# Kernel tuning notes

Hardware: AMD Instinct MI355X
Metric: run time of the kernel (lower is better)

Reference implementation:

```python
import jax, jax.numpy as jnp
import numpy as np
import math

N = 50000   # nodes
E = 800000  # edges
D = 128     # in/out dim
T = 4       # node types
H = 8       # heads (forced: Linear(8,64).view(-1, H, 8))
DK = D // H
HD = 8      # h_mat feature dim


def setup_inputs() -> dict:
    key = jax.random.key(0)
    ks = jax.random.split(key, 16)
    g = lambda k, shp, fan: jax.random.uniform(k, shp, jnp.float32, -1.0, 1.0) * math.sqrt(6.0 / fan)
    return {
        "meta_xs": jax.random.normal(ks[0], (N, D), jnp.float32),
        "node_type": jax.random.randint(ks[1], (N,), 0, T),
        "edge_index": jax.random.randint(ks[2], (2, E), 0, N),
        "h_mat": jax.random.normal(ks[3], (N, HD), jnp.float32),
        "sub_W": g(ks[4], (T, D, D), 2 * D),
        "sub_b": jnp.zeros((T, D), jnp.float32),
        "neigh_W": g(ks[5], (T, D, D), 2 * D),
        "neigh_b": jnp.zeros((T, D), jnp.float32),
        "hsub_W": g(ks[6], (HD, H * HD), HD + H * HD),
        "hsub_b": jnp.zeros((H * HD,), jnp.float32),
        "hneigh_W": g(ks[7], (HD, H * HD), HD + H * HD),
        "hneigh_b": jnp.zeros((H * HD,), jnp.float32),
        "relation_att": g(ks[8], (T, H, DK), H + DK),
        "relation_h_att": g(ks[9], (T, H, HD), H + HD),
        "ln_gamma": jnp.ones((D,), jnp.float32),
        "ln_beta": jnp.zeros((D,), jnp.float32),
    }


def _hgt_forward(meta_xs, h_mat, sub_W, sub_b, neigh_W, neigh_b, hsub_W, hsub_b,
                 hneigh_W, hneigh_b, relation_att, relation_h_att, ln_gamma, ln_beta,
                 node_type, edge_index):
    n = meta_xs.shape[0]
    e = edge_index.shape[1]
    src = edge_index[0]  # edge_index_j (neighbor)
    dst = edge_index[1]  # edge_index_i (sub / target)
    sqrt_dk = math.sqrt(DK)
    d_h = math.sqrt(H)

    # per-node, type-selected linear projections (sub by own type, neigh by own type)
    q_all = jnp.einsum('nd,tdo->tno', meta_xs, sub_W) + sub_b[:, None, :]      # [T,N,D]
    k_all = jnp.einsum('nd,tdo->tno', meta_xs, neigh_W) + neigh_b[:, None, :]  # [T,N,D]
    ar = jnp.arange(n)
    q_node = q_all[node_type, ar]  # [N,D] sub_linear[type_i](x_i)
    k_node = k_all[node_type, ar]  # [N,D] neigh_linear[type_j](x_j)

    h_sub_node = (h_mat @ hsub_W + hsub_b).reshape(n, H, HD)
    h_neigh_node = (h_mat @ hneigh_W + hneigh_b).reshape(n, H, HD)

    st = node_type[dst]  # sub type per edge selects relation params
    h_s = h_sub_node[dst]    # [E,H,8]
    h_n = h_neigh_node[src]  # [E,H,8]
    att_h = jnp.sum(jnp.tanh(h_s * h_n) * relation_h_att[st], axis=-1) / d_h  # [E,H]

    q_e = q_node[dst].reshape(e, H, DK)
    k_e = k_node[src].reshape(e, H, DK)
    att = jnp.sum(jnp.tanh(q_e * k_e) * relation_att[st], axis=-1) / sqrt_dk * att_h  # [E,H]

    # edge softmax over destination segments
    m = jax.ops.segment_max(att, dst, num_segments=n)  # [N,H]
    ea = jnp.exp(att - m[dst])
    denom = jax.ops.segment_sum(ea, dst, num_segments=n)
    alpha = ea / (denom[dst] + 1e-16)  # [E,H]

    msg = (k_e * alpha[:, :, None]).reshape(e, D)
    aggr = jax.ops.segment_sum(msg, dst, num_segments=n)  # [N,D]

    out = jax.nn.gelu(aggr, approximate=False)
    mu = jnp.mean(out, axis=-1, keepdims=True)
    var = jnp.var(out, axis=-1, keepdims=True)
    return (out - mu) * jax.lax.rsqrt(var + 1e-5) * ln_gamma + ln_beta


def reference(meta_xs, node_type, edge_index, h_mat, sub_W, sub_b, neigh_W, neigh_b,
              hsub_W, hsub_b, hneigh_W, hneigh_b, relation_att, relation_h_att,
              ln_gamma, ln_beta):
    return _hgt_forward(meta_xs, h_mat, sub_W, sub_b, neigh_W, neigh_b, hsub_W, hsub_b,
                        hneigh_W, hneigh_b, relation_att, relation_h_att, ln_gamma, ln_beta,
                        node_type, edge_index)
```

## Files before the change

kernel.cpp:

```cpp
#include <hip/hip_runtime.h>

typedef __bf16 bf16x8 __attribute__((ext_vector_type(8)));
typedef float f32x4 __attribute__((ext_vector_type(4)));

#define B_CHUNK 64
#define R_RANGE 2

__device__ __forceinline__ float exp2_fast(float x){
#if __has_builtin(__builtin_amdgcn_exp2f)
  return __builtin_amdgcn_exp2f(x);
#else
  return __expf(x * 0.69314718055994531f);
#endif
}
template<int CTRL>
__device__ __forceinline__ float dpp_add(float x){
  union { float f; int i; } a, b;
  a.f = x;
  b.i = __builtin_amdgcn_mov_dpp(a.i, CTRL, 0xF, 0xF, true);
  return x + b.f;
}
__device__ __forceinline__ float sum4(float x){
  x = dpp_add<0xB1>(x);
  x = dpp_add<0x4E>(x);
  return x;
}
__device__ __forceinline__ unsigned int cvt_pk_bf16(float lo, float hi){
  unsigned int r;
  asm("v_cvt_pk_bf16_f32 %0, %1, %2" : "=v"(r) : "v"(lo), "v"(hi));
  return r;
}
__device__ __forceinline__ unsigned short f2bf1(float f){
  return (unsigned short)cvt_pk_bf16(f, f);
}
__device__ __forceinline__ bf16x8 ld_bf8(const unsigned short* p){
  union { uint4 u; bf16x8 v; } c;
  c.u = *reinterpret_cast<const uint4*>(p);
  return c.v;
}
__device__ __forceinline__ bf16x8 ld_f32_to_bf8(const float* p){
  float4 lo = *reinterpret_cast<const float4*>(p);
  float4 hi = *reinterpret_cast<const float4*>(p + 4);
  union { unsigned int u[4]; bf16x8 v; } c;
  c.u[0] = cvt_pk_bf16(lo.x, lo.y);
  c.u[1] = cvt_pk_bf16(lo.z, lo.w);
  c.u[2] = cvt_pk_bf16(hi.x, hi.y);
  c.u[3] = cvt_pk_bf16(hi.z, hi.w);
  return c.v;
}

__global__ __launch_bounds__(256) void k_prep(const int* ntype, int* tcur, int* nbt,
                       int Npad, int N,
                       const float* subW, const float* neighW,
                       unsigned short* wts, unsigned short* wtn,
                       const int* ei, int E, unsigned short* hist,
                       unsigned short* rank, int RNG, int HR, int NB){
  __shared__ unsigned int lsh[12544];
  int b = blockIdx.x;
  const int SB1 = B_CHUNK * R_RANGE;
  if (b < SB1){
    int cb = b & (B_CHUNK - 1);
    int r  = b >> 6;
    int lo = r * RNG;
    int bins = RNG >> 1;
    for (int i = threadIdx.x; i < bins; i += 256) lsh[i] = 0;
    __syncthreads();
    int C = (E + B_CHUNK - 1) / B_CHUNK;
    int e0 = cb * C;
    int e1 = e0 + C; if (e1 > E) e1 = E;
    for (int i = e0 + threadIdx.x; i < e1; i += 256){
      int d = ei[E + i] - lo;
      if ((unsigned)d < (unsigned)RNG){
        unsigned old = atomicAdd(&lsh[d >> 1], (d & 1) ? 65536u : 1u);
        rank[i] = (unsigned short)((old >> ((d & 1) << 4)) & 0xffffu);
      }
    }
    __syncthreads();
    unsigned int* hrow = reinterpret_cast<unsigned int*>(hist + (size_t)cb*HR + lo);
    for (int i = threadIdx.x; i < bins; i += 256) hrow[i] = lsh[i];
  } else if (b < SB1 + NB){
    int i = (b - SB1)*256 + threadIdx.x;
    if (i >= N) return;
    int lane = threadIdx.x & 63;
    int myt = ntype[i];
    unsigned long long below = (lane == 0) ? 0ull : ((~0ull) >> (64 - lane));
    #pragma unroll
    for (int tt = 0; tt < 4; ++tt){
      unsigned long long mask = __ballot(myt == tt);
      if (mask){
        int leader = __ffsll((long long)mask) - 1;
        int base = 0;
        if (lane == leader) base = atomicAdd(&tcur[tt], __popcll(mask));
        base = __shfl(base, leader);
        if (myt == tt){
          int pos = base + __popcll(mask & below);
          nbt[tt*Npad + pos] = i;
        }
      }
    }
  } else {
    int i = (b - SB1 - NB)*256 + threadIdx.x;
    int w = i >> 16;
    int r = i & 65535;
    int t = r >> 14;
    int rem = r & 16383;
    int o = rem >> 7;
    int kd = rem & 127;
    const float* src = w ? neighW : subW;
    unsigned short* dstp = w ? wtn : wts;
    dstp[(t << 14) + (o << 7) + kd] = f2bf1(src[(t << 14) + (kd << 7) + o]);
  }
}

__global__ __launch_bounds__(256) void k_mid(unsigned short* hist, int HR,
                       int* deg, int N, int SCB,
                       const float* h_mat, const float* hsW, const float* hsb,
                       const float* hnW, const float* hnb,
                       float2* hs2, char* hnc){
  int b = blockIdx.x;
  if (b < SCB){
    int d = b*256 + threadIdx.x;
    if (d >= N) return;
    unsigned run = 0;
    #pragma unroll 4
    for (int c = 0; c < B_CHUNK; ++c){
      unsigned short* p = hist + (size_t)c*HR + d;
      unsigned v = *p;
      *p = (unsigned short)run;
      run += v;
    }
    deg[d] = (int)run;
  } else {
    int i = (b - SCB)*256 + threadIdx.x;
    if (i >= N*32) return;
    int n = i >> 5, l = i & 31;
    const float* hm = h_mat + (size_t)n*8;
    const float2* hsW2 = reinterpret_cast<const float2*>(hsW);
    const float2* hnW2 = reinterpret_cast<const float2*>(hnW);
    float s0=0.f, s1=0.f, n0=0.f, n1=0.f;
    #pragma unroll
    for (int d = 0; d < 8; ++d){
      float hv = hm[d];
      float2 ws2 = hsW2[d*32 + l];
      float2 wn2 = hnW2[d*32 + l];
      s0 += hv * ws2.x; s1 += hv * ws2.y;
      n0 += hv * wn2.x; n1 += hv * wn2.y;
    }
    float2 bs = reinterpret_cast<const float2*>(hsb)[l];
    float2 bn = reinterpret_cast<const float2*>(hnb)[l];
    hs2[(size_t)i] = make_float2(s0 + bs.x, s1 + bs.y);
    *reinterpret_cast<unsigned int*>(hnc + (size_t)n*128 + l*4)
        = cvt_pk_bf16(n0 + bn.x, n1 + bn.y);
  }
}

__global__ __launch_bounds__(256) void k_ms(const float* X,
      const unsigned short* wts, const unsigned short* wtn,
      const float* sub_b, const float* neigh_b,
      const int* nbt, const int* tcur, int Npad,
      float* q, char* kkc,
      const int* ei, unsigned short* bucket, int E,
      const unsigned short* hist, int HR, const unsigned short* rank, int MB){
  int b = blockIdx.x;
  if (b < MB){
    int t = -1, chunk = 0, acc = 0;
    #pragma unroll
    for (int tt = 0; tt < 4; ++tt){
      int cnt = tcur[tt];
      int nc = (cnt + 63) >> 6;
      if (t < 0 && b < acc + nc){ t = tt; chunk = b - acc; }
      acc += nc;
    }
    if (t < 0) return;
    int lane = threadIdx.x & 63;
    int w = threadIdx.x >> 6;
    int quad = lane >> 4, l16 = lane & 15;
    int cnt = tcur[t];
    int p = chunk*64 + w*16 + l16;
    bool ok = p < cnt;
    int nid = nbt[t*Npad + (ok ? p : 0)];
    bf16x8 xb[4];
    #pragma unroll
    for (int kk = 0; kk < 4; ++kk)
      xb[kk] = ld_f32_to_bf8(X + (size_t)nid*128 + kk*32 + quad*8);
    #pragma unroll
    for (int pj = 0; pj < 2; ++pj){
      const unsigned short* Wt = pj ? wtn : wts;
      const float* bias = pj ? neigh_b : sub_b;
      #pragma unroll
      for (int ot = 0; ot < 8; ++ot){
        f32x4 c = {0.f, 0.f, 0.f, 0.f};
        #pragma unroll
        for (int kk = 0; kk < 4; ++kk){
          bf16x8 wa = ld_bf8(Wt + ((size_t)t << 14) + ((size_t)(ot*16 + l16) << 7)
                                + kk*32 + quad*8);
          c = __builtin_amdgcn_mfma_f32_16x16x32_bf16(wa, xb[kk], c, 0, 0, 0);
        }
        int o0 = ot*16 + quad*4;
        float4 b4 = *reinterpret_cast<const float4*>(bias + t*128 + o0);
        if (ok){
          if (pj == 0){
            float4 v = make_float4(c[0]+b4.x, c[1]+b4.y, c[2]+b4.z, c[3]+b4.w);
            *reinterpret_cast<float4*>(q + (size_t)nid*128 + o0) = v;
          } else {
            uint2 pk;
            pk.x = cvt_pk_bf16(c[0]+b4.x, c[1]+b4.y);
            pk.y = cvt_pk_bf16(c[2]+b4.z, c[3]+b4.w);
            *reinterpret_cast<uint2*>(kkc + ((size_t)nid << 8) + (size_t)(o0 << 1)) = pk;
          }
        }
      }
    }
  } else {
    int sb = b - MB;
    int cb = sb >> 3;
    int sub = sb & 7;
    int C = (E + B_CHUNK - 1) / B_CHUNK;
    int seg = (C + 7) >> 3;
    int s0 = sub*seg;
    int s1 = s0 + seg; if (s1 > C) s1 = C;
    int e0 = cb*C + s0;
    int e1 = cb*C + s1; if (e1 > E) e1 = E;
    const unsigned short* hrow = hist + (size_t)cb*HR;
    for (int i = e0 + threadIdx.x; i < e1; i += 256){
      int d = ei[E + i];
      int pos = (int)hrow[d] + (int)rank[i];
      if (pos < 128) bucket[(size_t)d*128 + pos] = (unsigned short)ei[i];
    }
  }
}

__global__ __launch_bounds__(256) void k_edge(const float* q, const char* kkc,
      const char* hnc, const float2* hs2, const int* degA,
      const unsigned short* bucket, const int* ntype,
      const float* rel_att, const float* rel_h_att,
      const float* ln_g, const float* ln_b,
      float* out, int N){
  int wid = (blockIdx.x*blockDim.x + threadIdx.x) >> 6;
  if (wid >= N) return;
  int lane = threadIdx.x & 63;
  int l = lane & 31;
  int half = (lane >> 5) & 1;
  int t4 = l & 3, head = l >> 2;
  const float TLOG2E = 2.8853900817779268f;
  float4 qv = *reinterpret_cast<const float4*>(q + (size_t)wid*128 + l*4);
  float qe0 = qv.x*TLOG2E, qe1 = qv.y*TLOG2E, qe2 = qv.z*TLOG2E, qe3 = qv.w*TLOG2E;
  float2 hv = hs2[(size_t)wid*32 + l];
  float he0 = hv.x*TLOG2E, he1 = hv.y*TLOG2E;
  int st = ntype[wid];
  int rb = st*8 + head;
  float4 ra = *reinterpret_cast<const float4*>(rel_att + rb*16 + t4*4);
  float2 rh = *reinterpret_cast<const float2*>(rel_h_att + rb*8 + t4*2);
  float c0 = -0.5f*ra.x, c1 = -0.5f*ra.y, c2 = -0.5f*ra.z, c3 = -0.5f*ra.w;
  float cs = 0.25f*(ra.x + ra.y + ra.z + ra.w);
  const float HSC = 0.35355339059327373f * 1.4426950408889634f;
  float rh0 = rh.x*HSC, rh1 = rh.y*HSC;
  float ch0 = -2.f*rh0, ch1 = -2.f*rh1, chs = rh0 + rh1;
  float s = 0.f, a0 = 0.f, a1 = 0.f, a2 = 0.f, a3 = 0.f;

  int deg = __builtin_amdgcn_readfirstlane(degA[wid]);
  if (deg > 128) deg = 128;
  unsigned bkt = reinterpret_cast<const unsigned*>(bucket)[(size_t)wid*64 + lane];
  int niter = (deg + 1) >> 1;
  const char* kk_l = kkc + l*8;
  const char* hn_l = hnc + l*4;

  struct KH { uint2 k; unsigned h; };
  auto lp = [&](int g)->KH {
    int gg = g < niter ? g : 0;
    unsigned v = (unsigned)__builtin_amdgcn_readlane((int)bkt, gg);
    int sA = (int)(v & 0xffffu);
    int sB = (2*gg + 1 < deg) ? (int)(v >> 16) : sA;
    int sy = half ? sB : sA;
    KH r;
    r.k = *reinterpret_cast<const uint2*>(kk_l + ((size_t)(unsigned)sy << 8));
    r.h = *reinterpret_cast<const unsigned*>(hn_l + ((size_t)(unsigned)sy << 7));
    return r;
  };
  auto pr = [&](KH P, int g){
    union { unsigned u; float f; } k0,k1,k2,k3,h0,h1;
    k0.u = P.k.x << 16; k1.u = P.k.x & 0xffff0000u;
    k2.u = P.k.y << 16; k3.u = P.k.y & 0xffff0000u;
    h0.u = P.h << 16;   h1.u = P.h & 0xffff0000u;
    float e0 = exp2_fast(qe0*k0.f), e1 = exp2_fast(qe1*k1.f);
    float e2 = exp2_fast(qe2*k2.f), e3 = exp2_fast(qe3*k3.f);
    float f0 = exp2_fast(he0*h0.f), f1 = exp2_fast(he1*h1.f);
    float r0 = __builtin_amdgcn_rcpf(e0 + 1.f), r1 = __builtin_amdgcn_rcpf(e1 + 1.f);
    float r2 = __builtin_amdgcn_rcpf(e2 + 1.f), r3 = __builtin_amdgcn_rcpf(e3 + 1.f);
    float g0 = __builtin_amdgcn_rcpf(f0 + 1.f), g1 = __builtin_amdgcn_rcpf(f1 + 1.f);
    float pp = fmaf(c0,r0, fmaf(c1,r1, fmaf(c2,r2, fmaf(c3,r3, cs))));
    float ph = fmaf(ch0,g0, fmaf(ch1,g1, chs));
    pp = sum4(pp);
    ph = sum4(ph);
    float w = exp2_fast(pp * ph);
    w = (2*g + half < deg) ? w : 0.f;
    s += w;
    a0 = fmaf(w, k0.f, a0); a1 = fmaf(w, k1.f, a1);
    a2 = fmaf(w, k2.f, a2); a3 = fmaf(w, k3.f, a3);
  };

  if (niter > 0){
    KH A = lp(0);
    KH B = lp(1);
    for (int g = 0; g < niter; g += 2){
      KH C = lp(g+2);
      pr(A, g);
      KH D = lp(g+3);
      if (g+1 < niter) pr(B, g+1);
      A = C; B = D;
    }
  }
  s  += __shfl_xor(s, 32);
  a0 += __shfl_xor(a0, 32); a1 += __shfl_xor(a1, 32);
  a2 += __shfl_xor(a2, 32); a3 += __shfl_xor(a3, 32);

  float inv = 1.0f / (s + 1e-16f);
  float x0 = a0*inv, x1 = a1*inv, x2 = a2*inv, x3 = a3*inv;
  const float IS2 = 0.70710678118654752f;
  x0 = 0.5f*x0*(1.f + erff(x0*IS2));
  x1 = 0.5f*x1*(1.f + erff(x1*IS2));
  x2 = 0.5f*x2*(1.f + erff(x2*IS2));
  x3 = 0.5f*x3*(1.f + erff(x3*IS2));
  float sm = x0+x1+x2+x3;
  float sq = x0*x0 + x1*x1 + x2*x2 + x3*x3;
  #pragma unroll
  for (int d = 1; d < 32; d <<= 1){ sm += __shfl_xor(sm, d); sq += __shfl_xor(sq, d); }
  float mu = sm * (1.f/128.f);
  float var = fmaxf(sq * (1.f/128.f) - mu*mu, 0.f);
  float r = rsqrtf(var + 1e-5f);
  if (half == 0){
    float4 g4 = *reinterpret_cast<const float4*>(ln_g + l*4);
    float4 b4 = *reinterpret_cast<const float4*>(ln_b + l*4);
    float4 o4 = make_float4((x0-mu)*r*g4.x + b4.x, (x1-mu)*r*g4.y + b4.y,
                            (x2-mu)*r*g4.z + b4.z, (x3-mu)*r*g4.w + b4.w);
    *reinterpret_cast<float4*>(out + (size_t)wid*128 + l*4) = o4;
  }
}

extern "C" void kernel_launch(void* const* d_in, const int* in_sizes, int n_in,
                              void* d_out, int out_size, void* d_ws, size_t ws_size,
                              hipStream_t stream) {
  const float* meta_xs  = (const float*)d_in[0];
  const int*   node_type= (const int*)d_in[1];
  const int*   edge_idx = (const int*)d_in[2];
  const float* h_mat    = (const float*)d_in[3];
  const float* sub_W    = (const float*)d_in[4];
  const float* sub_b    = (const float*)d_in[5];
  const float* neigh_W  = (const float*)d_in[6];
  const float* neigh_b  = (const float*)d_in[7];
  const float* hsub_W   = (const float*)d_in[8];
  const float* hsub_b   = (const float*)d_in[9];
  const float* hneigh_W = (const float*)d_in[10];
  const float* hneigh_b = (const float*)d_in[11];
  const float* rel_att  = (const float*)d_in[12];
  const float* rel_hatt = (const float*)d_in[13];
  const float* ln_g     = (const float*)d_in[14];
  const float* ln_b     = (const float*)d_in[15];

  const int N = in_sizes[0] / 128;
  const int E = in_sizes[2] / 2;
  const int Npad = (N + 63) & ~63;
  const int RNG = (((N + R_RANGE - 1) / R_RANGE) + 1) & ~1;
  const int HR  = RNG * R_RANGE;

  char* wbase = (char*)d_ws;
  size_t o = 0;
  auto carve = [&](size_t bytes)->char* {
    char* p = wbase + o;
    o = (o + bytes + 255) & ~(size_t)255;
    return p;
  };
  float*          q      = (float*)carve((size_t)N*128*4);
  char*           kkc    = carve((size_t)N*256);
  char*           hnc    = carve((size_t)N*128);
  float2*         hs2    = (float2*)carve((size_t)N*32*8);
  unsigned short* bucket = (unsigned short*)carve((size_t)N*128*2);
  unsigned short* hist   = (unsigned short*)carve((size_t)B_CHUNK*HR*2);
  unsigned short* rank   = (unsigned short*)carve((size_t)E*2);
  int*            deg    = (int*)carve((size_t)N*4);
  int*            tmeta  = (int*)carve(64);
  int*            nbt    = (int*)carve((size_t)4*Npad*4);
  unsigned short* wts    = (unsigned short*)carve((size_t)4*128*128*2);
  unsigned short* wtn    = (unsigned short*)carve((size_t)4*128*128*2);
  if (o > ws_size) return;

  int* tcur = tmeta;

  const int SB1 = B_CHUNK * R_RANGE;
  const int NB  = (N + 255) / 256;
  const int WB  = (2*4*128*128) / 256;
  const int SCB = (N + 255) / 256;
  const int HB  = (N*32 + 255) / 256;
  const int MB  = ((N + 63) >> 6) + 4;
  const int SB3 = B_CHUNK * 8;

  hipMemsetAsync(tmeta, 0, 64, stream);
  k_prep <<<SB1 + NB + WB, 256, 0, stream>>>(node_type, tcur, nbt, Npad, N,
                                       sub_W, neigh_W, wts, wtn,
                                       edge_idx, E, hist, rank, RNG, HR, NB);
  k_mid  <<<SCB + HB, 256, 0, stream>>>(hist, HR, deg, N, SCB,
                                       h_mat, hsub_W, hsub_b, hneigh_W, hneigh_b,
                                       hs2, hnc);
  k_ms   <<<MB + SB3, 256, 0, stream>>>(meta_xs, wts, wtn, sub_b, neigh_b,
                                       nbt, tcur, Npad, q, kkc,
                                       edge_idx, bucket, E, hist, HR, rank, MB);
  k_edge <<<(N+3)/4, 256, 0, stream>>>(q, kkc, hnc, hs2, deg, bucket, node_type,
                                       rel_att, rel_hatt, ln_g, ln_b,
                                       (float*)d_out, N);
}
```

Baseline: 291.8 us.

## Fuse preprocessing kernels into one cooperative persistent kernel with grid syncs

Merges the three preprocessing launches and the memset into a single cooperative kernel of 768 blocks. Work is rebalanced across phases separated by grid-wide syncs, and type bucketing moves to after the histogram phase. R_RANGE goes from 2 to 4 so the histogram shared buffer halves, which allows more blocks to be resident for a cooperative launch. The aim is to cut launch gaps and tail effects, at the cost of grid-sync overhead and more histogram passes over the edges. Separate kernels remain as a fallback if the cooperative launch fails.

```diff
diff --git a/kernel.cpp b/kernel.cpp
--- a/kernel.cpp
+++ b/kernel.cpp
@@ -1,10 +1,14 @@
 #include <hip/hip_runtime.h>
+#include <hip/hip_cooperative_groups.h>
+
+namespace cg = cooperative_groups;
 
 typedef __bf16 bf16x8 __attribute__((ext_vector_type(8)));
 typedef float f32x4 __attribute__((ext_vector_type(4)));
 
 #define B_CHUNK 64
-#define R_RANGE 2
+#define R_RANGE 4
+#define GRID_F 768
 
 __device__ __forceinline__ float exp2_fast(float x){
 #if __has_builtin(__builtin_amdgcn_exp2f)
@@ -49,186 +53,216 @@
   return c.v;
 }
 
-__global__ __launch_bounds__(256) void k_prep(const int* ntype, int* tcur, int* nbt,
-                       int Npad, int N,
-                       const float* subW, const float* neighW,
-                       unsigned short* wts, unsigned short* wtn,
-                       const int* ei, int E, unsigned short* hist,
-                       unsigned short* rank, int RNG, int HR, int NB){
-  __shared__ unsigned int lsh[12544];
-  int b = blockIdx.x;
+struct FArgs {
+  const int* ntype; int* tcur; int* nbt; int Npad; int N;
+  const float* subW; const float* neighW;
+  unsigned short* wts; unsigned short* wtn;
+  const int* ei; int E;
+  unsigned short* hist; unsigned short* rank; int RNG; int HR;
+  const float* h_mat; const float* hsW; const float* hsb;
+  const float* hnW; const float* hnb;
+  float2* hs2; char* hnc;
+  const float* X; const float* sub_b; const float* neigh_b;
+  float* q; char* kkc;
+  unsigned short* bucket; int* deg;
+};
+
+__device__ void phaseA(const FArgs& a, int bid, int nb){
+  __shared__ unsigned int lsh[6272];
   const int SB1 = B_CHUNK * R_RANGE;
-  if (b < SB1){
-    int cb = b & (B_CHUNK - 1);
-    int r  = b >> 6;
-    int lo = r * RNG;
-    int bins = RNG >> 1;
-    for (int i = threadIdx.x; i < bins; i += 256) lsh[i] = 0;
-    __syncthreads();
-    int C = (E + B_CHUNK - 1) / B_CHUNK;
-    int e0 = cb * C;
-    int e1 = e0 + C; if (e1 > E) e1 = E;
-    for (int i = e0 + threadIdx.x; i < e1; i += 256){
-      int d = ei[E + i] - lo;
-      if ((unsigned)d < (unsigned)RNG){
-        unsigned old = atomicAdd(&lsh[d >> 1], (d & 1) ? 65536u : 1u);
-        rank[i] = (unsigned short)((old >> ((d & 1) << 4)) & 0xffffu);
+  const int WB  = 512;
+  const int HB  = (a.N*32 + 255) >> 8;
+  const int TA  = SB1 + WB + HB;
+  if (bid == 0 && threadIdx.x < 4) a.tcur[threadIdx.x] = 0;
+  for (int t = bid; t < TA; t += nb){
+    if (t < SB1){
+      int cb = t & (B_CHUNK - 1);
+      int r  = t >> 6;
+      int lo = r * a.RNG;
+      int bins = a.RNG >> 1;
+      __syncthreads();
+      for (int i = threadIdx.x; i < bins; i += 256) lsh[i] = 0;
+      __syncthreads();
+      int C = (a.E + B_CHUNK - 1) / B_CHUNK;
+      int e0 = cb * C;
+      int e1 = e0 + C; if (e1 > a.E) e1 = a.E;
+      for (int i = e0 + threadIdx.x; i < e1; i += 256){
+        int d = a.ei[a.E + i] - lo;
+        if ((unsigned)d < (unsigned)a.RNG){
+          unsigned old = atomicAdd(&lsh[d >> 1], (d & 1) ? 65536u : 1u);
+          a.rank[i] = (unsigned short)((old >> ((d & 1) << 4)) & 0xffffu);
+        }
+      }
+      __syncthreads();
+      unsigned int* hrow =
+          reinterpret_cast<unsigned int*>(a.hist + (size_t)cb*a.HR + lo);
+      for (int i = threadIdx.x; i < bins; i += 256) hrow[i] = lsh[i];
+      __syncthreads();
+    } else if (t < SB1 + WB){
+      int i = (t - SB1)*256 + threadIdx.x;
+      int w = i >> 16;
+      int r = i & 65535;
+      int tt = r >> 14;
+      int rem = r & 16383;
+      int o = rem >> 7;
+      int kd = rem & 127;
+      const float* src = w ? a.neighW : a.subW;
+      unsigned short* dstp = w ? a.wtn : a.wts;
+      dstp[(tt << 14) + (o << 7) + kd] = f2bf1(src[(tt << 14) + (kd << 7) + o]);
+    } else {
+      int i = (t - SB1 - WB)*256 + threadIdx.x;
+      if (i < a.N*32){
+        int n = i >> 5, l = i & 31;
+        const float* hm = a.h_mat + (size_t)n*8;
+        const float2* hsW2 = reinterpret_cast<const float2*>(a.hsW);
+        const float2* hnW2 = reinterpret_cast<const float2*>(a.hnW);
+        float s0=0.f, s1=0.f, n0=0.f, n1=0.f;
+        #pragma unroll
+        for (int d = 0; d < 8; ++d){
+          float hv = hm[d];
+          float2 ws2 = hsW2[d*32 + l];
+          float2 wn2 = hnW2[d*32 + l];
+          s0 += hv * ws2.x; s1 += hv * ws2.y;
+          n0 += hv * wn2.x; n1 += hv * wn2.y;
+        }
+        float2 bs = reinterpret_cast<const float2*>(a.hsb)[l];
+        float2 bn = reinterpret_cast<const float2*>(a.hnb)[l];
+        a.hs2[(size_t)i] = make_float2(s0 + bs.x, s1 + bs.y);
+        *reinterpret_cast<unsigned int*>(a.hnc + (size_t)n*128 + l*4)
+            = cvt_pk_bf16(n0 + bn.x, n1 + bn.y);
       }
     }
-    __syncthreads();
-    unsigned int* hrow = reinterpret_cast<unsigned int*>(hist + (size_t)cb*HR + lo);
-    for (int i = threadIdx.x; i < bins; i += 256) hrow[i] = lsh[i];
-  } else if (b < SB1 + NB){
-    int i = (b - SB1)*256 + threadIdx.x;
-    if (i >= N) return;
-    int lane = threadIdx.x & 63;
-    int myt = ntype[i];
-    unsigned long long below = (lane == 0) ? 0ull : ((~0ull) >> (64 - lane));
-    #pragma unroll
-    for (int tt = 0; tt < 4; ++tt){
-      unsigned long long mask = __ballot(myt == tt);
-      if (mask){
-        int leader = __ffsll((long long)mask) - 1;
-        int base = 0;
-        if (lane == leader) base = atomicAdd(&tcur[tt], __popcll(mask));
-        base = __shfl(base, leader);
-        if (myt == tt){
-          int pos = base + __popcll(mask & below);
-          nbt[tt*Npad + pos] = i;
+  }
+}
+
+__device__ void phaseB(const FArgs& a, int bid, int nb){
+  const int SCB = (a.N + 255) >> 8;
+  const int TB  = SCB * 2;
+  for (int t = bid; t < TB; t += nb){
+    if (t < SCB){
+      int d = t*256 + threadIdx.x;
+      if (d < a.N){
+        unsigned run = 0;
+        #pragma unroll 4
+        for (int c = 0; c < B_CHUNK; ++c){
+          unsigned short* p = a.hist + (size_t)c*a.HR + d;
+          unsigned v = *p;
+          *p = (unsigned short)run;
+          run += v;
         }
-      }
-    }
-  } else {
-    int i = (b - SB1 - NB)*256 + threadIdx.x;
-    int w = i >> 16;
-    int r = i & 65535;
-    int t = r >> 14;
-    int rem = r & 16383;
-    int o = rem >> 7;
-    int kd = rem & 127;
-    const float* src = w ? neighW : subW;
-    unsigned short* dstp = w ? wtn : wts;
-    dstp[(t << 14) + (o << 7) + kd] = f2bf1(src[(t << 14) + (kd << 7) + o]);
-  }
-}
-
-__global__ __launch_bounds__(256) void k_mid(unsigned short* hist, int HR,
-                       int* deg, int N, int SCB,
-                       const float* h_mat, const float* hsW, const float* hsb,
-                       const float* hnW, const float* hnb,
-                       float2* hs2, char* hnc){
-  int b = blockIdx.x;
-  if (b < SCB){
-    int d = b*256 + threadIdx.x;
-    if (d >= N) return;
-    unsigned run = 0;
-    #pragma unroll 4
-    for (int c = 0; c < B_CHUNK; ++c){
-      unsigned short* p = hist + (size_t)c*HR + d;
-      unsigned v = *p;
-      *p = (unsigned short)run;
-      run += v;
-    }
-    deg[d] = (int)run;
-  } else {
-    int i = (b - SCB)*256 + threadIdx.x;
-    if (i >= N*32) return;
-    int n = i >> 5, l = i & 31;
-    const float* hm = h_mat + (size_t)n*8;
-    const float2* hsW2 = reinterpret_cast<const float2*>(hsW);
-    const float2* hnW2 = reinterpret_cast<const float2*>(hnW);
-    float s0=0.f, s1=0.f, n0=0.f, n1=0.f;
-    #pragma unroll
-    for (int d = 0; d < 8; ++d){
-      float hv = hm[d];
-      float2 ws2 = hsW2[d*32 + l];
-      float2 wn2 = hnW2[d*32 + l];
-      s0 += hv * ws2.x; s1 += hv * ws2.y;
-      n0 += hv * wn2.x; n1 += hv * wn2.y;
-    }
-    float2 bs = reinterpret_cast<const float2*>(hsb)[l];
-    float2 bn = reinterpret_cast<const float2*>(hnb)[l];
-    hs2[(size_t)i] = make_float2(s0 + bs.x, s1 + bs.y);
-    *reinterpret_cast<unsigned int*>(hnc + (size_t)n*128 + l*4)
-        = cvt_pk_bf16(n0 + bn.x, n1 + bn.y);
-  }
-}
-
-__global__ __launch_bounds__(256) void k_ms(const float* X,
-      const unsigned short* wts, const unsigned short* wtn,
-      const float* sub_b, const float* neigh_b,
-      const int* nbt, const int* tcur, int Npad,
-      float* q, char* kkc,
-      const int* ei, unsigned short* bucket, int E,
-      const unsigned short* hist, int HR, const unsigned short* rank, int MB){
-  int b = blockIdx.x;
-  if (b < MB){
-    int t = -1, chunk = 0, acc = 0;
-    #pragma unroll
-    for (int tt = 0; tt < 4; ++tt){
-      int cnt = tcur[tt];
-      int nc = (cnt + 63) >> 6;
-      if (t < 0 && b < acc + nc){ t = tt; chunk = b - acc; }
-      acc += nc;
-    }
-    if (t < 0) return;
-    int lane = threadIdx.x & 63;
-    int w = threadIdx.x >> 6;
-    int quad = lane >> 4, l16 = lane & 15;
-    int cnt = tcur[t];
-    int p = chunk*64 + w*16 + l16;
-    bool ok = p < cnt;
-    int nid = nbt[t*Npad + (ok ? p : 0)];
-    bf16x8 xb[4];
-    #pragma unroll
-    for (int kk = 0; kk < 4; ++kk)
-      xb[kk] = ld_f32_to_bf8(X + (size_t)nid*128 + kk*32 + quad*8);
-    #pragma unroll
-    for (int pj = 0; pj < 2; ++pj){
-      const unsigned short* Wt = pj ? wtn : wts;
-      const float* bias = pj ? neigh_b : sub_b;
-      #pragma unroll
-      for (int ot = 0; ot < 8; ++ot){
-        f32x4 c = {0.f, 0.f, 0.f, 0.f};
+        a.deg[d] = (int)run;
+      }
+    } else {
+      int i = (t - SCB)*256 + threadIdx.x;
+      if (i < a.N){
+        int lane = threadIdx.x & 63;
+        int myt = a.ntype[i];
+        unsigned long long below = (lane == 0) ? 0ull : ((~0ull) >> (64 - lane));
         #pragma unroll
-        for (int kk = 0; kk < 4; ++kk){
-          bf16x8 wa = ld_bf8(Wt + ((size_t)t << 14) + ((size_t)(ot*16 + l16) << 7)
-                                + kk*32 + quad*8);
-          c = __builtin_amdgcn_mfma_f32_16x16x32_bf16(wa, xb[kk], c, 0, 0, 0);
-        }
-        int o0 = ot*16 + quad*4;
-        float4 b4 = *reinterpret_cast<const float4*>(bias + t*128 + o0);
-        if (ok){
-          if (pj == 0){
-            float4 v = make_float4(c[0]+b4.x, c[1]+b4.y, c[2]+b4.z, c[3]+b4.w);
-            *reinterpret_cast<float4*>(q + (size_t)nid*128 + o0) = v;
-          } else {
-            uint2 pk;
-            pk.x = cvt_pk_bf16(c[0]+b4.x, c[1]+b4.y);
-            pk.y = cvt_pk_bf16(c[2]+b4.z, c[3]+b4.w);
-            *reinterpret_cast<uint2*>(kkc + ((size_t)nid << 8) + (size_t)(o0 << 1)) = pk;
+        for (int tt = 0; tt < 4; ++tt){
+          unsigned long long mask = __ballot(myt == tt);
+          if (mask){
+            int leader = __ffsll((long long)mask) - 1;
+            int base = 0;
+            if (lane == leader) base = atomicAdd(&a.tcur[tt], __popcll(mask));
+            base = __shfl(base, leader);
+            if (myt == tt){
+              int pos = base + __popcll(mask & below);
+              a.nbt[tt*a.Npad + pos] = i;
+            }
           }
         }
       }
     }
-  } else {
-    int sb = b - MB;
-    int cb = sb >> 3;
-    int sub = sb & 7;
-    int C = (E + B_CHUNK - 1) / B_CHUNK;
-    int seg = (C + 7) >> 3;
-    int s0 = sub*seg;
-    int s1 = s0 + seg; if (s1 > C) s1 = C;
-    int e0 = cb*C + s0;
-    int e1 = cb*C + s1; if (e1 > E) e1 = E;
-    const unsigned short* hrow = hist + (size_t)cb*HR;
-    for (int i = e0 + threadIdx.x; i < e1; i += 256){
-      int d = ei[E + i];
-      int pos = (int)hrow[d] + (int)rank[i];
-      if (pos < 128) bucket[(size_t)d*128 + pos] = (unsigned short)ei[i];
+  }
+}
+
+__device__ void phaseC(const FArgs& a, int bid, int nb){
+  const int SB3 = 512;
+  const int MBX = ((a.N + 63) >> 6) + 4;
+  const int TC  = SB3 + MBX;
+  for (int t = bid; t < TC; t += nb){
+    if (t < SB3){
+      int cb = t >> 3;
+      int sub = t & 7;
+      int C = (a.E + B_CHUNK - 1) / B_CHUNK;
+      int seg = (C + 7) >> 3;
+      int s0 = sub*seg;
+      int s1 = s0 + seg; if (s1 > C) s1 = C;
+      int e0 = cb*C + s0;
+      int e1 = cb*C + s1; if (e1 > a.E) e1 = a.E;
+      const unsigned short* hrow = a.hist + (size_t)cb*a.HR;
+      for (int i = e0 + threadIdx.x; i < e1; i += 256){
+        int d = a.ei[a.E + i];
+        int pos = (int)hrow[d] + (int)a.rank[i];
+        if (pos < 128) a.bucket[(size_t)d*128 + pos] = (unsigned short)a.ei[i];
+      }
+    } else {
+      int b = t - SB3;
+      int ts = -1, chunk = 0, acc = 0;
+      #pragma unroll
+      for (int tt = 0; tt < 4; ++tt){
+        int cnt = a.tcur[tt];
+        int nc = (cnt + 63) >> 6;
+        if (ts < 0 && b < acc + nc){ ts = tt; chunk = b - acc; }
+        acc += nc;
+      }
+      if (ts >= 0){
+        int lane = threadIdx.x & 63;
+        int w = threadIdx.x >> 6;
+        int quad = lane >> 4, l16 = lane & 15;
+        int cnt = a.tcur[ts];
+        int p = chunk*64 + w*16 + l16;
+        bool ok = p < cnt;
+        int nid = a.nbt[ts*a.Npad + (ok ? p : 0)];
+        bf16x8 xb[4];
+        #pragma unroll
+        for (int kk = 0; kk < 4; ++kk)
+          xb[kk] = ld_f32_to_bf8(a.X + (size_t)nid*128 + kk*32 + quad*8);
+        #pragma unroll
+        for (int pj = 0; pj < 2; ++pj){
+          const unsigned short* Wt = pj ? a.wtn : a.wts;
+          const float* bias = pj ? a.neigh_b : a.sub_b;
+          #pragma unroll
+          for (int ot = 0; ot < 8; ++ot){
+            f32x4 c = {0.f, 0.f, 0.f, 0.f};
+            #pragma unroll
+            for (int kk = 0; kk < 4; ++kk){
+              bf16x8 wa = ld_bf8(Wt + ((size_t)ts << 14) + ((size_t)(ot*16 + l16) << 7)
+                                    + kk*32 + quad*8);
+              c = __builtin_amdgcn_mfma_f32_16x16x32_bf16(wa, xb[kk], c, 0, 0, 0);
+            }
+            int o0 = ot*16 + quad*4;
+            float4 b4 = *reinterpret_cast<const float4*>(bias + ts*128 + o0);
+            if (ok){
+              if (pj == 0){
+                float4 v = make_float4(c[0]+b4.x, c[1]+b4.y, c[2]+b4.z, c[3]+b4.w);
+                *reinterpret_cast<float4*>(a.q + (size_t)nid*128 + o0) = v;
+              } else {
+                uint2 pk;
+                pk.x = cvt_pk_bf16(c[0]+b4.x, c[1]+b4.y);
+                pk.y = cvt_pk_bf16(c[2]+b4.z, c[3]+b4.w);
+                *reinterpret_cast<uint2*>(a.kkc + ((size_t)nid << 8) + (size_t)(o0 << 1)) = pk;
+              }
+            }
+          }
+        }
+      }
     }
   }
 }
+
+__global__ __launch_bounds__(256) void k_all(FArgs a){
+  cg::grid_group g = cg::this_grid();
+  phaseA(a, blockIdx.x, gridDim.x);
+  g.sync();
+  phaseB(a, blockIdx.x, gridDim.x);
+  g.sync();
+  phaseC(a, blockIdx.x, gridDim.x);
+}
+__global__ __launch_bounds__(256) void kA(FArgs a){ phaseA(a, blockIdx.x, gridDim.x); }
+__global__ __launch_bounds__(256) void kB(FArgs a){ phaseB(a, blockIdx.x, gridDim.x); }
+__global__ __launch_bounds__(256) void kC(FArgs a){ phaseC(a, blockIdx.x, gridDim.x); }
 
 __global__ __launch_bounds__(256) void k_edge(const float* q, const char* kkc,
       const char* hnc, const float2* hs2, const int* degA,
@@ -384,27 +418,28 @@
   unsigned short* wtn    = (unsigned short*)carve((size_t)4*128*128*2);
   if (o > ws_size) return;
 
-  int* tcur = tmeta;
-
-  const int SB1 = B_CHUNK * R_RANGE;
-  const int NB  = (N + 255) / 256;
-  const int WB  = (2*4*128*128) / 256;
-  const int SCB = (N + 255) / 256;
-  const int HB  = (N*32 + 255) / 256;
-  const int MB  = ((N + 63) >> 6) + 4;
-  const int SB3 = B_CHUNK * 8;
-
-  hipMemsetAsync(tmeta, 0, 64, stream);
-  k_prep <<<SB1 + NB + WB, 256, 0, stream>>>(node_type, tcur, nbt, Npad, N,
-                                       sub_W, neigh_W, wts, wtn,
-                                       edge_idx, E, hist, rank, RNG, HR, NB);
-  k_mid  <<<SCB + HB, 256, 0, stream>>>(hist, HR, deg, N, SCB,
-                                       h_mat, hsub_W, hsub_b, hneigh_W, hneigh_b,
-                                       hs2, hnc);
-  k_ms   <<<MB + SB3, 256, 0, stream>>>(meta_xs, wts, wtn, sub_b, neigh_b,
-                                       nbt, tcur, Npad, q, kkc,
-                                       edge_idx, bucket, E, hist, HR, rank, MB);
-  k_edge <<<(N+3)/4, 256, 0, stream>>>(q, kkc, hnc, hs2, deg, bucket, node_type,
-                                       rel_att, rel_hatt, ln_g, ln_b,
-                                       (float*)d_out, N);
-}
+  FArgs fa;
+  fa.ntype = node_type; fa.tcur = tmeta; fa.nbt = nbt; fa.Npad = Npad; fa.N = N;
+  fa.subW = sub_W; fa.neighW = neigh_W; fa.wts = wts; fa.wtn = wtn;
+  fa.ei = edge_idx; fa.E = E;
+  fa.hist = hist; fa.rank = rank; fa.RNG = RNG; fa.HR = HR;
+  fa.h_mat = h_mat; fa.hsW = hsub_W; fa.hsb = hsub_b;
+  fa.hnW = hneigh_W; fa.hnb = hneigh_b;
+  fa.hs2 = hs2; fa.hnc = hnc;
+  fa.X = meta_xs; fa.sub_b = sub_b; fa.neigh_b = neigh_b;
+  fa.q = q; fa.kkc = kkc;
+  fa.bucket = bucket; fa.deg = deg;
+
+  void* params[1] = { (void*)&fa };
+  hipError_t err = hipLaunchCooperativeKernel(
+      reinterpret_cast<void*>(k_all), dim3(GRID_F), dim3(256), params, 0, stream);
+  if (err != hipSuccess){
+    (void)hipGetLastError();
+    kA<<<GRID_F, 256, 0, stream>>>(fa);
+    kB<<<GRID_F, 256, 0, stream>>>(fa);
+    kC<<<GRID_F, 256, 0, stream>>>(fa);
+  }
+  k_edge<<<(N+3)/4, 256, 0, stream>>>(q, kkc, hnc, hs2, deg, bucket, node_type,
+                                      rel_att, rel_hatt, ln_g, ln_b,
+                                      (float*)d_out, N);
+}
```

New measurement: 475.9 us. 1.63x slower.
